# Kernel tuning notes

Hardware: AMD Instinct MI355X
Metric: run time of the kernel (lower is better)

Reference implementation:

```python
import jax, jax.numpy as jnp
import numpy as np

B, N, H = 2, 2048, 1024
NUM_HEADS, HEAD_DIM = 16, 64
SCALE = HEAD_DIM ** -0.5


def setup_inputs() -> dict:
    key = jax.random.key(0)
    ks = jax.random.split(key, 9)
    hidden_states = jax.random.normal(ks[0], (B, N, H), dtype=jnp.float32)
    # ancestor-only mask: lower-triangular incl. diagonal (chain tree)
    tree_mask = jnp.tril(jnp.ones((N, N), dtype=jnp.int32))
    s = H ** -0.5
    Wq = jax.random.normal(ks[1], (H, NUM_HEADS * HEAD_DIM), dtype=jnp.float32) * s
    Wk = jax.random.normal(ks[2], (H, NUM_HEADS * HEAD_DIM), dtype=jnp.float32) * s
    Wv = jax.random.normal(ks[3], (H, NUM_HEADS * HEAD_DIM), dtype=jnp.float32) * s
    Wo = jax.random.normal(ks[4], (NUM_HEADS * HEAD_DIM, H), dtype=jnp.float32) * s
    bq = jnp.zeros((NUM_HEADS * HEAD_DIM,), dtype=jnp.float32)
    bk = jnp.zeros((NUM_HEADS * HEAD_DIM,), dtype=jnp.float32)
    bv = jnp.zeros((NUM_HEADS * HEAD_DIM,), dtype=jnp.float32)
    bo = jnp.zeros((H,), dtype=jnp.float32)
    return {"hidden_states": hidden_states, "tree_mask": tree_mask,
            "Wq": Wq, "bq": bq, "Wk": Wk, "bk": bk,
            "Wv": Wv, "bv": bv, "Wo": Wo, "bo": bo}


def reference(hidden_states, tree_mask, Wq, bq, Wk, bk, Wv, bv, Wo, bo):
    b, n, _ = hidden_states.shape
    q = (hidden_states @ Wq + bq).reshape(b, n, NUM_HEADS, HEAD_DIM)
    k = (hidden_states @ Wk + bk).reshape(b, n, NUM_HEADS, HEAD_DIM)
    v = (hidden_states @ Wv + bv).reshape(b, n, NUM_HEADS, HEAD_DIM)
    # scores: [b, heads, n, n]
    scores = jnp.einsum('bqhd,bkhd->bhqk', q, k) * SCALE
    neg_inf = jnp.finfo(scores.dtype).min
    scores = jnp.where(tree_mask[None, None, :, :] == 0, neg_inf, scores)
    attn = jax.nn.softmax(scores, axis=-1)  # dropout p=0.0 -> identity
    out = jnp.einsum('bhqk,bkhd->bqhd', attn, v).reshape(b, n, NUM_HEADS * HEAD_DIM)
    return out @ Wo + bo
```

## Files before the change

kernel.cpp:

```cpp
#include <hip/hip_runtime.h>
#include <hip/hip_bf16.h>
#include <stdint.h>

typedef unsigned short u16;
typedef short short8 __attribute__((ext_vector_type(8)));
typedef float f32x4 __attribute__((ext_vector_type(4)));
typedef u16 u16x4 __attribute__((ext_vector_type(4)));

#define SCLOG 0.18033688011112042f

static __device__ __forceinline__ u16 f2bf(float f) {
  unsigned u = __float_as_uint(f);
  unsigned rnd = 0x7fffu + ((u >> 16) & 1u);
  return (u16)((u + rnd) >> 16);
}

static __device__ __forceinline__ unsigned pk_bf16(float a, float b) {
  unsigned r;
  asm("v_cvt_pk_bf16_f32 %0, %1, %2" : "=v"(r) : "v"(a), "v"(b));
  return r;
}

static __device__ __forceinline__ void gload_lds16(const void* g, void* l) {
  __builtin_amdgcn_global_load_lds(
      (const __attribute__((address_space(1))) unsigned int*)g,
      (__attribute__((address_space(3))) unsigned int*)l, 16, 0, 0);
}

__global__ __launch_bounds__(256) void prep_kernel(
    const float* __restrict__ hs, const int* __restrict__ mask,
    const float* __restrict__ Wq, const float* __restrict__ Wk,
    const float* __restrict__ Wv, const float* __restrict__ Wo,
    u16* __restrict__ X, u16* __restrict__ WT,
    unsigned long long* __restrict__ bits) {
  __shared__ float tile[32][33];
  const int bid = blockIdx.x;
  const int tid = threadIdx.x;
  if (bid < 4096) {
    const int i = bid * 256 + tid;
    const float4 v = reinterpret_cast<const float4*>(hs)[i];
    u16x4 o;
    o[0] = f2bf(v.x); o[1] = f2bf(v.y); o[2] = f2bf(v.z); o[3] = f2bf(v.w);
    reinterpret_cast<u16x4*>(X)[i] = o;
  } else if (bid < 8192) {
    const int B = bid - 4096;
    const int z = B >> 10, y = (B >> 5) & 31, x = B & 31;
    const float* src = (z == 0) ? Wq : (z == 1) ? Wk : (z == 2) ? Wv : Wo;
    u16* dst = WT + (size_t)z * 1024 * 1024;
    const int row0 = y * 32, col0 = x * 32;
    const int tx = tid & 31, ty = tid >> 5;
#pragma unroll
    for (int i = 0; i < 4; ++i)
      tile[ty + i * 8][tx] = src[(size_t)(row0 + ty + i * 8) * 1024 + col0 + tx];
    __syncthreads();
#pragma unroll
    for (int i = 0; i < 4; ++i) {
      const int r = ty + i * 8;
      dst[(size_t)(col0 + r) * 1024 + row0 + tx] = f2bf(tile[tx][r]);
    }
  } else {
    const int gw = (bid - 8192) * 4 + (tid >> 6);
    const int lane = tid & 63;
    const int q = gw >> 5, w = gw & 31;
    const int mv = mask[(size_t)q * 2048 + w * 64 + lane];
    const unsigned long long bal = __ballot(mv != 0);
    if (lane == 0) bits[(size_t)q * 32 + w] = bal;
  }
}

__global__ __launch_bounds__(256) void gemm_qkv_kernel(
    const u16* __restrict__ X, const u16* __restrict__ WT,
    const float* __restrict__ bq, const float* __restrict__ bk, const float* __restrict__ bv,
    u16* __restrict__ Qb, u16* __restrict__ Kb, u16* __restrict__ Vb) {
  __shared__ u16 As[128 * 32];
  __shared__ u16 Bs[128 * 32];
  const int tid = threadIdx.x;
  const int lane = tid & 63, wid = tid >> 6;
  const int l15 = lane & 15, lg = lane >> 4;
  const int n0 = blockIdx.x * 128, m0 = blockIdx.y * 128;
  const int wr = wid >> 1, wc = wid & 1;

  f32x4 acc[4][4] = {};

  for (int kt = 0; kt < 32; ++kt) {
    __syncthreads();
#pragma unroll
    for (int p = 0; p < 2; ++p) {
      const int c = p * 256 + tid;
      const int r = c >> 2, ch = c & 3;
      gload_lds16(X + (size_t)(m0 + r) * 1024 + kt * 32 + ch * 8,
                  &As[(p * 256 + wid * 64) * 8]);
      gload_lds16(WT + (size_t)(n0 + r) * 1024 + kt * 32 + ch * 8,
                  &Bs[(p * 256 + wid * 64) * 8]);
    }
    __syncthreads();
    short8 af[4], bfr[4];
#pragma unroll
    for (int i = 0; i < 4; ++i) {
      af[i] = *reinterpret_cast<const short8*>(&As[(wr * 64 + i * 16 + l15) * 32 + lg * 8]);
      bfr[i] = *reinterpret_cast<const short8*>(&Bs[(wc * 64 + i * 16 + l15) * 32 + lg * 8]);
    }
#pragma unroll
    for (int i = 0; i < 4; ++i)
#pragma unroll
      for (int j = 0; j < 4; ++j)
        acc[i][j] = __builtin_amdgcn_mfma_f32_16x16x32_bf16(bfr[j], af[i], acc[i][j], 0, 0, 0);
  }

#pragma unroll
  for (int i = 0; i < 4; ++i) {
    const int m = m0 + wr * 64 + i * 16 + l15;
    const int bb = m >> 11, t = m & 2047;
#pragma unroll
    for (int j = 0; j < 4; ++j) {
      const int n = n0 + wc * 64 + j * 16 + lg * 4;
      const float* bsrc = (n < 1024) ? (bq + n) : (n < 2048) ? (bk + n - 1024) : (bv + n - 2048);
      const float4 b4 = *reinterpret_cast<const float4*>(bsrc);
      const float scl = (n < 1024) ? SCLOG : 1.0f;
      u16* dst = (n < 1024) ? Qb : (n < 2048) ? Kb : Vb;
      const int nl = n & 1023;
      const int hh = nl >> 6, d0 = nl & 63;
      uint2 pk;
      pk.x = pk_bf16((acc[i][j][0] + b4.x) * scl, (acc[i][j][1] + b4.y) * scl);
      pk.y = pk_bf16((acc[i][j][2] + b4.z) * scl, (acc[i][j][3] + b4.w) * scl);
      *reinterpret_cast<uint2*>(dst + ((size_t)(bb * 16 + hh) * 2048 + t) * 64 + d0) = pk;
    }
  }
}

__global__ __launch_bounds__(256) void transpose_v_kernel(const u16* __restrict__ Vb,
                                                          u16* __restrict__ VT) {
  __shared__ u16 tile[64][68];
  const int tid = threadIdx.x;
  const int tt = blockIdx.x & 31;
  const int bh = blockIdx.x >> 5;
  const size_t base = (size_t)bh * 2048 * 64;
  const int t0 = tt * 64;
#pragma unroll
  for (int p = 0; p < 2; ++p) {
    int i = p * 256 + tid;
    int row = i >> 3, ch = i & 7;
    *reinterpret_cast<short8*>(&tile[row][ch * 8]) =
        *reinterpret_cast<const short8*>(Vb + base + (size_t)(t0 + row) * 64 + ch * 8);
  }
  __syncthreads();
#pragma unroll
  for (int p = 0; p < 2; ++p) {
    int i = p * 256 + tid;
    int d = i >> 3, ch = i & 7;
    short8 v;
#pragma unroll
    for (int j = 0; j < 8; ++j) v[j] = tile[ch * 8 + j][d];
    *reinterpret_cast<short8*>(VT + base + (size_t)d * 2048 + t0 + ch * 8) = v;
  }
}

struct AttnState {
  f32x4 O[4];
  float m, l;
  short8 qf0, qf1;
};

static __device__ __forceinline__ void attn_tile(
    AttnState& st, const u16* __restrict__ Kb_, const u16* __restrict__ Vb_,
    u16* __restrict__ pwave, unsigned long long w,
    int l15, int lg, int slg) {
  f32x4 sT[4] = {};
  __builtin_amdgcn_s_setprio(1);
#pragma unroll
  for (int dc = 0; dc < 2; ++dc) {
    const short8 qv = dc ? st.qf1 : st.qf0;
#pragma unroll
    for (int sub = 0; sub < 4; ++sub) {
      const short8 kf = *reinterpret_cast<const short8*>(
          &Kb_[dc * 2048 + (sub * 16 + l15) * 32 + slg]);
      sT[sub] = __builtin_amdgcn_mfma_f32_16x16x32_bf16(kf, qv, sT[sub], 0, 0, 0);
    }
  }
  __builtin_amdgcn_s_setprio(0);

  if (!__all(w == ~0ull)) {
    const unsigned mlo = (unsigned)w, mhi = (unsigned)(w >> 32);
#pragma unroll
    for (int sub = 0; sub < 4; ++sub) {
      const unsigned f = ((sub & 2) ? mhi : mlo) >> ((sub & 1) * 16 + lg * 4);
#pragma unroll
      for (int r = 0; r < 4; ++r)
        sT[sub][r] = ((f >> r) & 1u) ? sT[sub][r] : -1e30f;
    }
  }
  float pm;
  {
    const float t0 = fmaxf(fmaxf(sT[0][0], sT[0][1]), fmaxf(sT[0][2], sT[0][3]));
    const float t1 = fmaxf(fmaxf(sT[1][0], sT[1][1]), fmaxf(sT[1][2], sT[1][3]));
    const float t2 = fmaxf(fmaxf(sT[2][0], sT[2][1]), fmaxf(sT[2][2], sT[2][3]));
    const float t3 = fmaxf(fmaxf(sT[3][0], sT[3][1]), fmaxf(sT[3][2], sT[3][3]));
    pm = fmaxf(fmaxf(t0, t1), fmaxf(t2, t3));
  }
  pm = fmaxf(pm, __shfl_xor(pm, 16));
  pm = fmaxf(pm, __shfl_xor(pm, 32));
  if (!__all(pm - st.m <= 8.f)) {
    const float mn = fmaxf(st.m, pm);
    const float al = exp2f(st.m - mn);
    st.m = mn;
    st.l *= al;
#pragma unroll
    for (int dt = 0; dt < 4; ++dt) st.O[dt] *= al;
  }

  float lsum = 0.f;
#pragma unroll
  for (int kc = 0; kc < 2; ++kc) {
#pragma unroll
    for (int s2 = 0; s2 < 2; ++s2) {
      const int sub = kc * 2 + s2;
      const float e0 = exp2f(sT[sub][0] - st.m);
      const float e1 = exp2f(sT[sub][1] - st.m);
      const float e2 = exp2f(sT[sub][2] - st.m);
      const float e3 = exp2f(sT[sub][3] - st.m);
      lsum += (e0 + e1) + (e2 + e3);
      uint2 pk;
      pk.x = pk_bf16(e0, e1);
      pk.y = pk_bf16(e2, e3);
      *reinterpret_cast<uint2*>(&pwave[l15 * 40 + s2 * 16 + lg * 4]) = pk;
    }
    const short8 pf = *reinterpret_cast<const short8*>(&pwave[l15 * 40 + lg * 8]);
    __builtin_amdgcn_s_setprio(1);
#pragma unroll
    for (int dt = 0; dt < 4; ++dt) {
      const short8 vf = *reinterpret_cast<const short8*>(
          &Vb_[kc * 2048 + (dt * 16 + l15) * 32 + slg]);
      st.O[dt] = __builtin_amdgcn_mfma_f32_16x16x32_bf16(vf, pf, st.O[dt], 0, 0, 0);
    }
    __builtin_amdgcn_s_setprio(0);
  }
  st.l += lsum;
}

__global__ __launch_bounds__(256, 4) void attn_kernel(
    const u16* __restrict__ Q, const u16* __restrict__ K, const u16* __restrict__ VT,
    const unsigned long long* __restrict__ MB, u16* __restrict__ AO) {
  __shared__ u16 K_lds[2][4096];
  __shared__ u16 V_lds[2][4096];
  __shared__ u16 p_lds[4][16][40];
  __shared__ unsigned actA_s, actB_s;

  const int tid = threadIdx.x;
  const int wid = tid >> 6, lane = tid & 63;
  const int l15 = lane & 15, lg = lane >> 4;

  const int wgid = blockIdx.x;
  const int x = wgid & 7, s = wgid >> 3;
  const int g = x + 8 * (s >> 5);
  const int qp = s & 31;
  const int h = g & 15, b = g >> 4;
  const int qA_t = qp, qB_t = 63 - qp;
  const size_t bh_off = ((size_t)(b * 16 + h)) * 2048 * 64;

  if (tid == 0) { actA_s = 0; actB_s = 0; }
  __syncthreads();
  {
    const int ktc = tid & 31, rg = tid >> 5;
    unsigned long long orA = 0, orB = 0;
#pragma unroll
    for (int i = 0; i < 4; ++i) {
      orA |= MB[(size_t)(qA_t * 32 + rg * 4 + i) * 32 + ktc];
      orB |= MB[(size_t)(qB_t * 32 + rg * 4 + i) * 32 + ktc];
    }
    if (orA) atomicOr(&actA_s, 1u << ktc);
    if (orB) atomicOr(&actB_s, 1u << ktc);
  }

  const int sid = wid >> 1;
  const int qt = sid ? qB_t : qA_t;
  const int q = qt * 32 + (wid & 1) * 16 + l15;

  AttnState st;
  {
    const short8* qp_ = reinterpret_cast<const short8*>(Q + bh_off + (size_t)q * 64);
    st.qf0 = qp_[lg]; st.qf1 = qp_[4 + lg];
#pragma unroll
    for (int dt = 0; dt < 4; ++dt) st.O[dt] = f32x4{};
    st.m = -3e38f; st.l = 0.f;
  }

  const int slg = (lg ^ ((l15 >> 1) & 3)) * 8;

  int offK[2], offV[2], ldsi[2];
#pragma unroll
  for (int p = 0; p < 2; ++p) {
    const int i = wid * 128 + p * 64 + lane;
    const int pc = i >> 8, row = (i >> 2) & 63, lgc = i & 3;
    const int lgs = lgc ^ ((i >> 3) & 3);
    offK[p] = row * 64 + pc * 32 + lgs * 8;
    offV[p] = row * 2048 + pc * 32 + lgs * 8;
    ldsi[p] = (wid * 128 + p * 64) * 8;
  }
  const u16* Kg = K + bh_off;
  const u16* Vg = VT + bh_off;
  u16* pwave = &p_lds[wid][0][0];

  __syncthreads();
  const unsigned actA = actA_s, actB = actB_s;
  const unsigned actW = sid ? actB : actA;
  unsigned rem = actA | actB;
  int buf = 0;

#define STAGE_TILE(bb, ktv)                                        \
  do {                                                             \
    const u16* ksrc_ = Kg + (ktv) * 64 * 64;                       \
    const u16* vsrc_ = Vg + (ktv) * 64;                            \
    _Pragma("unroll") for (int p_ = 0; p_ < 2; ++p_) {             \
      gload_lds16(ksrc_ + offK[p_], &K_lds[bb][ldsi[p_]]);         \
      gload_lds16(vsrc_ + offV[p_], &V_lds[bb][ldsi[p_]]);         \
    }                                                              \
  } while (0)

  if (rem) {
    int kt = __ffs(rem) - 1;
    unsigned long long w_cur = MB[(size_t)q * 32 + kt];
    STAGE_TILE(0, kt);
    __syncthreads();

    while (true) {
      rem &= rem - 1;
      int ktn = -1;
      unsigned long long w_next = 0;
      if (rem) {
        ktn = __ffs(rem) - 1;
        w_next = MB[(size_t)q * 32 + ktn];
        STAGE_TILE(buf ^ 1, ktn);
      }

      if ((actW >> kt) & 1u)
        attn_tile(st, &K_lds[buf][0], &V_lds[buf][0], pwave, w_cur, l15, lg, slg);

      if (ktn < 0) break;
      __syncthreads();
      buf ^= 1;
      kt = ktn;
      w_cur = w_next;
    }
  }
#undef STAGE_TILE

  {
    float lr = st.l;
    lr += __shfl_xor(lr, 16);
    lr += __shfl_xor(lr, 32);
    const float inv = (lr > 0.f) ? (1.0f / lr) : 0.f;
    u16* dst = AO + ((size_t)(b * 2048 + q)) * 1024 + h * 64;
#pragma unroll
    for (int dt = 0; dt < 4; ++dt) {
      uint2 pk;
      pk.x = pk_bf16(st.O[dt][0] * inv, st.O[dt][1] * inv);
      pk.y = pk_bf16(st.O[dt][2] * inv, st.O[dt][3] * inv);
      *reinterpret_cast<uint2*>(dst + dt * 16 + lg * 4) = pk;
    }
  }
}

__global__ __launch_bounds__(256) void gemm_out_kernel(
    const u16* __restrict__ A, const u16* __restrict__ BT,
    const float* __restrict__ bo, float* __restrict__ out) {
  __shared__ u16 As[128 * 32];
  __shared__ u16 Bs[128 * 32];
  const int tid = threadIdx.x;
  const int lane = tid & 63, wid = tid >> 6;
  const int l15 = lane & 15, lg = lane >> 4;
  const int n0 = blockIdx.x * 128, m0 = blockIdx.y * 128;
  const int wr = wid >> 1, wc = wid & 1;

  f32x4 acc[4][4] = {};

  for (int kt = 0; kt < 32; ++kt) {
    __syncthreads();
#pragma unroll
    for (int p = 0; p < 2; ++p) {
      const int c = p * 256 + tid;
      const int r = c >> 2, ch = c & 3;
      gload_lds16(A + (size_t)(m0 + r) * 1024 + kt * 32 + ch * 8,
                  &As[(p * 256 + wid * 64) * 8]);
      gload_lds16(BT + (size_t)(n0 + r) * 1024 + kt * 32 + ch * 8,
                  &Bs[(p * 256 + wid * 64) * 8]);
    }
    __syncthreads();
    short8 af[4], bfr[4];
#pragma unroll
    for (int i = 0; i < 4; ++i) {
      af[i] = *reinterpret_cast<const short8*>(&As[(wr * 64 + i * 16 + l15) * 32 + lg * 8]);
      bfr[i] = *reinterpret_cast<const short8*>(&Bs[(wc * 64 + i * 16 + l15) * 32 + lg * 8]);
    }
#pragma unroll
    for (int i = 0; i < 4; ++i)
#pragma unroll
      for (int j = 0; j < 4; ++j)
        acc[i][j] = __builtin_amdgcn_mfma_f32_16x16x32_bf16(bfr[j], af[i], acc[i][j], 0, 0, 0);
  }

#pragma unroll
  for (int i = 0; i < 4; ++i) {
    const int m = m0 + wr * 64 + i * 16 + l15;
#pragma unroll
    for (int j = 0; j < 4; ++j) {
      const int n = n0 + wc * 64 + j * 16 + lg * 4;
      const float4 b4 = *reinterpret_cast<const float4*>(bo + n);
      float4 o4;
      o4.x = acc[i][j][0] + b4.x;
      o4.y = acc[i][j][1] + b4.y;
      o4.z = acc[i][j][2] + b4.z;
      o4.w = acc[i][j][3] + b4.w;
      *reinterpret_cast<float4*>(out + (size_t)m * 1024 + n) = o4;
    }
  }
}

extern "C" void kernel_launch(void* const* d_in, const int* in_sizes, int n_in,
                              void* d_out, int out_size, void* d_ws, size_t ws_size,
                              hipStream_t stream) {
  (void)in_sizes; (void)n_in; (void)out_size; (void)ws_size;
  const float* hs = (const float*)d_in[0];
  const int* mask = (const int*)d_in[1];
  const float* Wq = (const float*)d_in[2];
  const float* bq = (const float*)d_in[3];
  const float* Wk = (const float*)d_in[4];
  const float* bk = (const float*)d_in[5];
  const float* Wv = (const float*)d_in[6];
  const float* bv = (const float*)d_in[7];
  const float* Wo = (const float*)d_in[8];
  const float* bo = (const float*)d_in[9];
  float* out = (float*)d_out;

  uint8_t* ws = (uint8_t*)d_ws;
  u16* X  = (u16*)(ws);
  u16* WT = (u16*)(ws + ((size_t)8 << 20));
  u16* Qb = (u16*)(ws + ((size_t)16 << 20));
  u16* Kb = (u16*)(ws + ((size_t)24 << 20));
  u16* Vb = (u16*)(ws + ((size_t)32 << 20));
  u16* AO = (u16*)(ws + ((size_t)40 << 20));
  unsigned long long* MB = (unsigned long long*)(ws + ((size_t)48 << 20));
  u16* VbT = X;

  prep_kernel<<<dim3(24576), dim3(256), 0, stream>>>(hs, mask, Wq, Wk, Wv, Wo, X, WT, MB);
  gemm_qkv_kernel<<<dim3(24, 32), dim3(256), 0, stream>>>(X, WT, bq, bk, bv, Qb, Kb, Vb);
  transpose_v_kernel<<<dim3(1024), dim3(256), 0, stream>>>(Vb, VbT);
  attn_kernel<<<dim3(1024), dim3(256), 0, stream>>>(Qb, Kb, VbT, MB, AO);
  gemm_out_kernel<<<dim3(8, 32), dim3(256), 0, stream>>>(AO, WT + (size_t)3072 * 1024, bo, out);
}
```

Before: 143.6 us.

## Read K/V directly from global memory per wave, dropping LDS staging

The attention kernel no longer double-buffers K and V^T tiles in shared memory with block-wide barriers. Each wave now owns one 16-row query tile, builds its own active-key-tile mask with a ballot, and loads K and V fragments straight from global memory, relying on L2/L1 caching. This removes the __syncthreads, the LDS staging and the block-level mask reduction, and lets waves run independently. The cost is more global and cache traffic, because K/V are no longer shared across the four waves, and no explicit prefetch hides load latency.

```diff
diff --git a/kernel.cpp b/kernel.cpp
--- a/kernel.cpp
+++ b/kernel.cpp
@@ -161,21 +161,25 @@
   short8 qf0, qf1;
 };
 
-static __device__ __forceinline__ void attn_tile(
-    AttnState& st, const u16* __restrict__ Kb_, const u16* __restrict__ Vb_,
-    u16* __restrict__ pwave, unsigned long long w,
-    int l15, int lg, int slg) {
+static __device__ __forceinline__ void attn_tile_g(
+    AttnState& st, const u16* __restrict__ Kt, const u16* __restrict__ Vt,
+    u16* __restrict__ pwave, unsigned long long w, int l15, int lg) {
+  short8 kf[2][4];
+#pragma unroll
+  for (int dc = 0; dc < 2; ++dc)
+#pragma unroll
+    for (int sub = 0; sub < 4; ++sub)
+      kf[dc][sub] = *reinterpret_cast<const short8*>(
+          Kt + (size_t)(sub * 16 + l15) * 64 + dc * 32 + lg * 8);
+
   f32x4 sT[4] = {};
   __builtin_amdgcn_s_setprio(1);
 #pragma unroll
   for (int dc = 0; dc < 2; ++dc) {
     const short8 qv = dc ? st.qf1 : st.qf0;
 #pragma unroll
-    for (int sub = 0; sub < 4; ++sub) {
-      const short8 kf = *reinterpret_cast<const short8*>(
-          &Kb_[dc * 2048 + (sub * 16 + l15) * 32 + slg]);
-      sT[sub] = __builtin_amdgcn_mfma_f32_16x16x32_bf16(kf, qv, sT[sub], 0, 0, 0);
-    }
+    for (int sub = 0; sub < 4; ++sub)
+      sT[sub] = __builtin_amdgcn_mfma_f32_16x16x32_bf16(kf[dc][sub], qv, sT[sub], 0, 0, 0);
   }
   __builtin_amdgcn_s_setprio(0);
 
@@ -229,7 +233,7 @@
 #pragma unroll
     for (int dt = 0; dt < 4; ++dt) {
       const short8 vf = *reinterpret_cast<const short8*>(
-          &Vb_[kc * 2048 + (dt * 16 + l15) * 32 + slg]);
+          Vt + (size_t)(dt * 16 + l15) * 2048 + kc * 32 + lg * 8);
       st.O[dt] = __builtin_amdgcn_mfma_f32_16x16x32_bf16(vf, pf, st.O[dt], 0, 0, 0);
     }
     __builtin_amdgcn_s_setprio(0);
@@ -240,10 +244,7 @@
 __global__ __launch_bounds__(256, 4) void attn_kernel(
     const u16* __restrict__ Q, const u16* __restrict__ K, const u16* __restrict__ VT,
     const unsigned long long* __restrict__ MB, u16* __restrict__ AO) {
-  __shared__ u16 K_lds[2][4096];
-  __shared__ u16 V_lds[2][4096];
   __shared__ u16 p_lds[4][16][40];
-  __shared__ unsigned actA_s, actB_s;
 
   const int tid = threadIdx.x;
   const int wid = tid >> 6, lane = tid & 63;
@@ -252,28 +253,11 @@
   const int wgid = blockIdx.x;
   const int x = wgid & 7, s = wgid >> 3;
   const int g = x + 8 * (s >> 5);
-  const int qp = s & 31;
+  const int p = s & 31;
   const int h = g & 15, b = g >> 4;
-  const int qA_t = qp, qB_t = 63 - qp;
+  const int qt = (wid == 0) ? p : (wid == 1) ? 63 - p : (wid == 2) ? 64 + p : 127 - p;
+  const int q = qt * 16 + l15;
   const size_t bh_off = ((size_t)(b * 16 + h)) * 2048 * 64;
-
-  if (tid == 0) { actA_s = 0; actB_s = 0; }
-  __syncthreads();
-  {
-    const int ktc = tid & 31, rg = tid >> 5;
-    unsigned long long orA = 0, orB = 0;
-#pragma unroll
-    for (int i = 0; i < 4; ++i) {
-      orA |= MB[(size_t)(qA_t * 32 + rg * 4 + i) * 32 + ktc];
-      orB |= MB[(size_t)(qB_t * 32 + rg * 4 + i) * 32 + ktc];
-    }
-    if (orA) atomicOr(&actA_s, 1u << ktc);
-    if (orB) atomicOr(&actB_s, 1u << ktc);
-  }
-
-  const int sid = wid >> 1;
-  const int qt = sid ? qB_t : qA_t;
-  const int q = qt * 32 + (wid & 1) * 16 + l15;
 
   AttnState st;
   {
@@ -284,65 +268,26 @@
     st.m = -3e38f; st.l = 0.f;
   }
 
-  const int slg = (lg ^ ((l15 >> 1) & 3)) * 8;
-
-  int offK[2], offV[2], ldsi[2];
-#pragma unroll
-  for (int p = 0; p < 2; ++p) {
-    const int i = wid * 128 + p * 64 + lane;
-    const int pc = i >> 8, row = (i >> 2) & 63, lgc = i & 3;
-    const int lgs = lgc ^ ((i >> 3) & 3);
-    offK[p] = row * 64 + pc * 32 + lgs * 8;
-    offV[p] = row * 2048 + pc * 32 + lgs * 8;
-    ldsi[p] = (wid * 128 + p * 64) * 8;
-  }
+  unsigned rem;
+  {
+    const int c = lane & 31;
+    unsigned long long orw = 0;
+#pragma unroll
+    for (int i = 0; i < 16; ++i)
+      orw |= MB[(size_t)(qt * 16 + i) * 32 + c];
+    rem = (unsigned)__ballot(orw != 0);
+  }
+
   const u16* Kg = K + bh_off;
   const u16* Vg = VT + bh_off;
   u16* pwave = &p_lds[wid][0][0];
 
-  __syncthreads();
-  const unsigned actA = actA_s, actB = actB_s;
-  const unsigned actW = sid ? actB : actA;
-  unsigned rem = actA | actB;
-  int buf = 0;
-
-#define STAGE_TILE(bb, ktv)                                        \
-  do {                                                             \
-    const u16* ksrc_ = Kg + (ktv) * 64 * 64;                       \
-    const u16* vsrc_ = Vg + (ktv) * 64;                            \
-    _Pragma("unroll") for (int p_ = 0; p_ < 2; ++p_) {             \
-      gload_lds16(ksrc_ + offK[p_], &K_lds[bb][ldsi[p_]]);         \
-      gload_lds16(vsrc_ + offV[p_], &V_lds[bb][ldsi[p_]]);         \
-    }                                                              \
-  } while (0)
-
-  if (rem) {
-    int kt = __ffs(rem) - 1;
-    unsigned long long w_cur = MB[(size_t)q * 32 + kt];
-    STAGE_TILE(0, kt);
-    __syncthreads();
-
-    while (true) {
-      rem &= rem - 1;
-      int ktn = -1;
-      unsigned long long w_next = 0;
-      if (rem) {
-        ktn = __ffs(rem) - 1;
-        w_next = MB[(size_t)q * 32 + ktn];
-        STAGE_TILE(buf ^ 1, ktn);
-      }
-
-      if ((actW >> kt) & 1u)
-        attn_tile(st, &K_lds[buf][0], &V_lds[buf][0], pwave, w_cur, l15, lg, slg);
-
-      if (ktn < 0) break;
-      __syncthreads();
-      buf ^= 1;
-      kt = ktn;
-      w_cur = w_next;
-    }
-  }
-#undef STAGE_TILE
+  while (rem) {
+    const int kt = __ffs(rem) - 1;
+    rem &= rem - 1;
+    const unsigned long long w = MB[(size_t)q * 32 + kt];
+    attn_tile_g(st, Kg + (size_t)kt * 64 * 64, Vg + (size_t)kt * 64, pwave, w, l15, lg);
+  }
 
   {
     float lr = st.l;
```

Result: slower. 219.3 us (+52.7%).

## Deepen GEMM K-tiles to 64 with XOR-swizzled LDS and XCD-aware block mapping

Applied to the files above, without the earlier changes.

Both projection GEMMs now stage 64-wide K slices per iteration instead of 32, which halves the number of barrier pairs. The LDS chunk index is XOR-swizzled by row to avoid bank conflicts on the short8 fragment reads. The QKV GEMM uses a 1D grid that gives each XCD a contiguous group of N tiles, aiming for better L2 reuse of the weight tiles. Doubling the LDS footprint may reduce occupancy.

```diff
diff --git a/kernel.cpp b/kernel.cpp
--- a/kernel.cpp
+++ b/kernel.cpp
@@ -72,39 +72,49 @@
     const u16* __restrict__ X, const u16* __restrict__ WT,
     const float* __restrict__ bq, const float* __restrict__ bk, const float* __restrict__ bv,
     u16* __restrict__ Qb, u16* __restrict__ Kb, u16* __restrict__ Vb) {
-  __shared__ u16 As[128 * 32];
-  __shared__ u16 Bs[128 * 32];
+  __shared__ u16 As[128 * 64];
+  __shared__ u16 Bs[128 * 64];
   const int tid = threadIdx.x;
   const int lane = tid & 63, wid = tid >> 6;
   const int l15 = lane & 15, lg = lane >> 4;
-  const int n0 = blockIdx.x * 128, m0 = blockIdx.y * 128;
+  const int wg = blockIdx.x;
+  const int xcd = wg & 7, idx = wg >> 3;
+  const int n0 = (xcd * 3 + (idx >> 5)) * 128;
+  const int m0 = (idx & 31) * 128;
   const int wr = wid >> 1, wc = wid & 1;
 
   f32x4 acc[4][4] = {};
 
-  for (int kt = 0; kt < 32; ++kt) {
-    __syncthreads();
-#pragma unroll
-    for (int p = 0; p < 2; ++p) {
+  for (int kt = 0; kt < 16; ++kt) {
+    __syncthreads();
+#pragma unroll
+    for (int p = 0; p < 4; ++p) {
       const int c = p * 256 + tid;
-      const int r = c >> 2, ch = c & 3;
-      gload_lds16(X + (size_t)(m0 + r) * 1024 + kt * 32 + ch * 8,
+      const int row = c >> 3, sch = (c & 7) ^ (row & 7);
+      gload_lds16(X + (size_t)(m0 + row) * 1024 + kt * 64 + sch * 8,
                   &As[(p * 256 + wid * 64) * 8]);
-      gload_lds16(WT + (size_t)(n0 + r) * 1024 + kt * 32 + ch * 8,
+      gload_lds16(WT + (size_t)(n0 + row) * 1024 + kt * 64 + sch * 8,
                   &Bs[(p * 256 + wid * 64) * 8]);
     }
     __syncthreads();
-    short8 af[4], bfr[4];
-#pragma unroll
-    for (int i = 0; i < 4; ++i) {
-      af[i] = *reinterpret_cast<const short8*>(&As[(wr * 64 + i * 16 + l15) * 32 + lg * 8]);
-      bfr[i] = *reinterpret_cast<const short8*>(&Bs[(wc * 64 + i * 16 + l15) * 32 + lg * 8]);
-    }
-#pragma unroll
-    for (int i = 0; i < 4; ++i)
-#pragma unroll
-      for (int j = 0; j < 4; ++j)
-        acc[i][j] = __builtin_amdgcn_mfma_f32_16x16x32_bf16(bfr[j], af[i], acc[i][j], 0, 0, 0);
+#pragma unroll
+    for (int kk = 0; kk < 2; ++kk) {
+      short8 af[4], bfr[4];
+#pragma unroll
+      for (int i = 0; i < 4; ++i) {
+        const int ra = wr * 64 + i * 16 + l15;
+        af[i] = *reinterpret_cast<const short8*>(
+            &As[ra * 64 + ((kk * 4 + lg) ^ (ra & 7)) * 8]);
+        const int rb = wc * 64 + i * 16 + l15;
+        bfr[i] = *reinterpret_cast<const short8*>(
+            &Bs[rb * 64 + ((kk * 4 + lg) ^ (rb & 7)) * 8]);
+      }
+#pragma unroll
+      for (int i = 0; i < 4; ++i)
+#pragma unroll
+        for (int j = 0; j < 4; ++j)
+          acc[i][j] = __builtin_amdgcn_mfma_f32_16x16x32_bf16(bfr[j], af[i], acc[i][j], 0, 0, 0);
+    }
   }
 
 #pragma unroll
@@ -363,39 +373,48 @@
 __global__ __launch_bounds__(256) void gemm_out_kernel(
     const u16* __restrict__ A, const u16* __restrict__ BT,
     const float* __restrict__ bo, float* __restrict__ out) {
-  __shared__ u16 As[128 * 32];
-  __shared__ u16 Bs[128 * 32];
+  __shared__ u16 As[128 * 64];
+  __shared__ u16 Bs[128 * 64];
   const int tid = threadIdx.x;
   const int lane = tid & 63, wid = tid >> 6;
   const int l15 = lane & 15, lg = lane >> 4;
-  const int n0 = blockIdx.x * 128, m0 = blockIdx.y * 128;
+  const int wg = blockIdx.x;
+  const int n0 = (wg & 7) * 128;
+  const int m0 = (wg >> 3) * 128;
   const int wr = wid >> 1, wc = wid & 1;
 
   f32x4 acc[4][4] = {};
 
-  for (int kt = 0; kt < 32; ++kt) {
-    __syncthreads();
-#pragma unroll
-    for (int p = 0; p < 2; ++p) {
+  for (int kt = 0; kt < 16; ++kt) {
+    __syncthreads();
+#pragma unroll
+    for (int p = 0; p < 4; ++p) {
       const int c = p * 256 + tid;
-      const int r = c >> 2, ch = c & 3;
-      gload_lds16(A + (size_t)(m0 + r) * 1024 + kt * 32 + ch * 8,
+      const int row = c >> 3, sch = (c & 7) ^ (row & 7);
+      gload_lds16(A + (size_t)(m0 + row) * 1024 + kt * 64 + sch * 8,
                   &As[(p * 256 + wid * 64) * 8]);
-      gload_lds16(BT + (size_t)(n0 + r) * 1024 + kt * 32 + ch * 8,
+      gload_lds16(BT + (size_t)(n0 + row) * 1024 + kt * 64 + sch * 8,
                   &Bs[(p * 256 + wid * 64) * 8]);
     }
     __syncthreads();
-    short8 af[4], bfr[4];
-#pragma unroll
-    for (int i = 0; i < 4; ++i) {
-      af[i] = *reinterpret_cast<const short8*>(&As[(wr * 64 + i * 16 + l15) * 32 + lg * 8]);
-      bfr[i] = *reinterpret_cast<const short8*>(&Bs[(wc * 64 + i * 16 + l15) * 32 + lg * 8]);
-    }
-#pragma unroll
-    for (int i = 0; i < 4; ++i)
-#pragma unroll
-      for (int j = 0; j < 4; ++j)
-        acc[i][j] = __builtin_amdgcn_mfma_f32_16x16x32_bf16(bfr[j], af[i], acc[i][j], 0, 0, 0);
+#pragma unroll
+    for (int kk = 0; kk < 2; ++kk) {
+      short8 af[4], bfr[4];
+#pragma unroll
+      for (int i = 0; i < 4; ++i) {
+        const int ra = wr * 64 + i * 16 + l15;
+        af[i] = *reinterpret_cast<const short8*>(
+            &As[ra * 64 + ((kk * 4 + lg) ^ (ra & 7)) * 8]);
+        const int rb = wc * 64 + i * 16 + l15;
+        bfr[i] = *reinterpret_cast<const short8*>(
+            &Bs[rb * 64 + ((kk * 4 + lg) ^ (rb & 7)) * 8]);
+      }
+#pragma unroll
+      for (int i = 0; i < 4; ++i)
+#pragma unroll
+        for (int j = 0; j < 4; ++j)
+          acc[i][j] = __builtin_amdgcn_mfma_f32_16x16x32_bf16(bfr[j], af[i], acc[i][j], 0, 0, 0);
+    }
   }
 
 #pragma unroll
@@ -442,8 +461,8 @@
   u16* VbT = X;
 
   prep_kernel<<<dim3(24576), dim3(256), 0, stream>>>(hs, mask, Wq, Wk, Wv, Wo, X, WT, MB);
-  gemm_qkv_kernel<<<dim3(24, 32), dim3(256), 0, stream>>>(X, WT, bq, bk, bv, Qb, Kb, Vb);
+  gemm_qkv_kernel<<<dim3(768), dim3(256), 0, stream>>>(X, WT, bq, bk, bv, Qb, Kb, Vb);
   transpose_v_kernel<<<dim3(1024), dim3(256), 0, stream>>>(Vb, VbT);
   attn_kernel<<<dim3(1024), dim3(256), 0, stream>>>(Qb, Kb, VbT, MB, AO);
-  gemm_out_kernel<<<dim3(8, 32), dim3(256), 0, stream>>>(AO, WT + (size_t)3072 * 1024, bo, out);
-}
+  gemm_out_kernel<<<dim3(256), dim3(256), 0, stream>>>(AO, WT + (size_t)3072 * 1024, bo, out);
+}
```

New measurement: 154.2 us. +7.3%, slower.
